# Kernel optimization log

Hardware: AMD Instinct MI355X
Metric: run time of the kernel (lower is better)

## Reference

```python
import jax, jax.numpy as jnp
import numpy as np

T, N, E = 4, 20000, 320000
F_IN, EH, NH, GH, OUT = 12, 32, 64, 64, 1
NUM_LAYERS = 2
EB_IN = (EH + 2 * NH) * 2 + GH  # 384
NB_IN = 2 * NH + 2 * EH + GH    # 256
GB_IN = NH + EH + GH            # 160


def setup_inputs() -> dict:
    key = jax.random.key(0)
    ks = jax.random.split(key, 24)
    f32 = jnp.float32
    def w(k, fan_in, shape):
        return jax.random.normal(k, shape, f32) * (1.0 / np.sqrt(fan_in))
    return {
        "node_attr": jax.random.normal(ks[0], (T, N, F_IN), f32),
        "edge_attr": jax.random.normal(ks[1], (T, E, 1), f32),
        "edge_index": jax.random.randint(ks[2], (2, E), 0, N, jnp.int32),
        "sp_L_vals": jax.random.normal(ks[3], (E,), f32),
        "global_attr": jax.random.normal(ks[4], (1, GH), f32),
        "coeff": jnp.full((1,), 0.1, f32),
        "W_ee": w(ks[5], 1, (1, EH)), "b_ee": jnp.zeros((EH,), f32),
        "W_ne": w(ks[6], F_IN, (F_IN, NH)), "b_ne": jnp.zeros((NH,), f32),
        "W_eb": w(ks[7], EB_IN, (EB_IN, EH)), "b_eb": jnp.zeros((EH,), f32),
        "W_nb": w(ks[8], NB_IN, (NB_IN, NH)), "b_nb": jnp.zeros((NH,), f32),
        "W_gb": w(ks[9], GB_IN, (GB_IN, GH)), "b_gb": jnp.zeros((GH,), f32),
        "W_nd1": w(ks[10], NH, (NH, NH)), "b_nd1": jnp.zeros((NH,), f32),
        "W_nd2": w(ks[11], NH, (NH, OUT)), "b_nd2": jnp.zeros((OUT,), f32),
    }


def _forward(node_attr, edge_attr, edge_index, sp_L_vals, global_attr, coeff,
             W_ee, b_ee, W_ne, b_ne, W_eb, b_eb, W_nb, b_nb, W_gb, b_gb,
             W_nd1, b_nd1, W_nd2, b_nd2):
    relu = jax.nn.relu
    s, r = edge_index[0], edge_index[1]
    seg = lambda v, idx: jax.ops.segment_sum(v, idx, num_segments=N)
    c = coeff[0]

    # encoders
    x_enc = relu(node_attr @ W_ne + b_ne)   # [T,N,NH]
    e_enc = relu(edge_attr @ W_ee + b_ee)   # [T,E,EH]

    def run_gn(xT, eT, g0):
        # recurrent GN core over processing steps; hidden (h_x,h_e,h_g) starts at zeros
        def step(carry, inp):
            h_x, h_e, h_g = carry
            x_in, e_in = inp
            gE = jnp.broadcast_to(h_g, (E, GH))
            # EdgeBlock: [edge_in, edge_h, sender_in, sender_h, recv_in, recv_h, global]
            edge_cat = jnp.concatenate(
                [e_in, h_e, x_in[s], h_x[s], x_in[r], h_x[r], gE], axis=-1)
            e_new = relu(edge_cat @ W_eb + b_eb)              # [E,EH]
            sent = seg(e_new, s)                              # scatter_add by sender
            recv = seg(e_new, r)                              # scatter_add by receiver
            gN = jnp.broadcast_to(h_g, (N, GH))
            node_cat = jnp.concatenate([x_in, h_x, sent, recv, gN], axis=-1)
            x_new = relu(node_cat @ W_nb + b_nb)              # [N,NH]
            # GlobalBlock: scatter_mean == plain mean (single graph)
            g_cat = jnp.concatenate(
                [x_new.mean(0, keepdims=True), e_new.mean(0, keepdims=True), h_g], axis=-1)
            g_new = relu(g_cat @ W_gb + b_gb)                 # [1,GH]
            # physics terms (pde='diff'): time derivative = state update,
            # spatial derivative = coeff * (graph-Laplacian action via sp_L edge weights)
            t_der = x_new - h_x
            s_der = c * seg(sp_L_vals[:, None] * (x_new[s] - x_new[r]), r)
            return (x_new, e_new, g_new), (x_new, e_new, g_new, t_der, s_der)
        carry0 = (jnp.zeros((N, NH), jnp.float32), jnp.zeros((E, EH), jnp.float32), g0)
        _, ys = jax.lax.scan(step, carry0, (xT, eT))
        return ys  # xs[T,N,NH], es[T,E,EH], gs[T,1,GH], td[T,N,NH], sd[T,N,NH]

    xs, es, gs, td, sd = run_gn(x_enc, e_enc, global_attr)
    x_pre = x_enc
    for _ in range(NUM_LAYERS - 1):
        x_res = xs + x_pre          # residual node state feeds next GN layer
        x_pre = x_res
        xs, es, gs, td, sd = run_gn(x_res, es, gs[0])

    x_final = xs + x_pre            # add_residual=True final residual
    h = relu(x_final @ W_nd1 + b_nd1)
    out_nodes = h @ W_nd2 + b_nd2   # [T,N,OUT]
    return out_nodes, td, sd


def reference(node_attr, edge_attr, edge_index, sp_L_vals, global_attr, coeff,
              W_ee, b_ee, W_ne, b_ne, W_eb, b_eb, W_nb, b_nb, W_gb, b_gb,
              W_nd1, b_nd1, W_nd2, b_nd2):
    return _forward(node_attr, edge_attr, edge_index, sp_L_vals, global_attr, coeff,
                    W_ee, b_ee, W_ne, b_ne, W_eb, b_eb, W_nb, b_nb, W_gb, b_gb,
                    W_nd1, b_nd1, W_nd2, b_nd2)
```

## Files before the change

### kernel.cpp

```cpp
#include <hip/hip_runtime.h>


typedef __attribute__((ext_vector_type(8))) short s16x8;
typedef __attribute__((ext_vector_type(4))) float f32x4;

#define T_STEPS 4
#define NN 20000
#define NP 20224
#define NE 320000

__device__ __forceinline__ float bf2f(unsigned short h){
  return __uint_as_float(((unsigned)h)<<16);
}
__device__ __forceinline__ unsigned short f2bf(float f){
  unsigned u = __float_as_uint(f);
  return (unsigned short)((u + 0x7fffu + ((u>>16)&1u)) >> 16);
}
__device__ __forceinline__ float loadIn(const void* p, size_t i, int bf){
  return bf ? bf2f(((const unsigned short*)p)[i]) : ((const float*)p)[i];
}
__device__ __forceinline__ void storeOut(void* o, size_t i, float v, int bf){
  if(bf) ((unsigned short*)o)[i] = f2bf(v);
  else   ((float*)o)[i] = v;
}
__device__ __forceinline__ void load8(const float* __restrict__ p, float* v){
  const float4* q4 = (const float4*)p;
  float4 a = q4[0], b = q4[1];
  v[0]=a.x; v[1]=a.y; v[2]=a.z; v[3]=a.w;
  v[4]=b.x; v[5]=b.y; v[6]=b.z; v[7]=b.w;
}
__device__ __forceinline__ int4 pack8(const float* v){
  unsigned p0 = (unsigned)f2bf(v[0]) | ((unsigned)f2bf(v[1])<<16);
  unsigned p1 = (unsigned)f2bf(v[2]) | ((unsigned)f2bf(v[3])<<16);
  unsigned p2 = (unsigned)f2bf(v[4]) | ((unsigned)f2bf(v[5])<<16);
  unsigned p3 = (unsigned)f2bf(v[6]) | ((unsigned)f2bf(v[7])<<16);
  return make_int4((int)p0,(int)p1,(int)p2,(int)p3);
}
__device__ __forceinline__ void unp8(int4 w, float* a){
  unsigned x;
  x=(unsigned)w.x; a[0]=__uint_as_float(x<<16); a[1]=__uint_as_float(x&0xffff0000u);
  x=(unsigned)w.y; a[2]=__uint_as_float(x<<16); a[3]=__uint_as_float(x&0xffff0000u);
  x=(unsigned)w.z; a[4]=__uint_as_float(x<<16); a[5]=__uint_as_float(x&0xffff0000u);
  x=(unsigned)w.w; a[6]=__uint_as_float(x<<16); a[7]=__uint_as_float(x&0xffff0000u);
}

union I4S8 { int4 i; s16x8 s; };

__global__ void probe_kernel(const void* coeff_in, int* flagp, float* coeff_f){
  unsigned short u = ((const unsigned short*)coeff_in)[0];
  float as_bf = bf2f(u);
  int f = (fabsf(as_bf - 0.1f) < 0.02f) ? 1 : 0;
  *flagp = f;
  *coeff_f = f ? as_bf : ((const float*)coeff_in)[0];
}

struct ConvJob { const void* src; float* dst; int n; };
struct ConvJobs { ConvJob j[16]; int cnt; };

__global__ void conv_kernel(ConvJobs jobs, const int* flagp, float* z, int zn){
  int bf = *flagp;
  int tid = blockIdx.x*blockDim.x + threadIdx.x;
  int stride = gridDim.x*blockDim.x;
  for(int q=0;q<jobs.cnt;q++){
    const void* s = jobs.j[q].src; float* d = jobs.j[q].dst; int n = jobs.j[q].n;
    for(int i=tid;i<n;i+=stride) d[i] = loadIn(s, i, bf);
  }
  for(int i=tid;i<zn;i+=stride) z[i]=0.f;
}

__global__ void csr_hist(const int* __restrict__ ei, int* deg_s, int* deg_r,
                         unsigned short* __restrict__ rank_s,
                         unsigned short* __restrict__ rank_r){
  int e = blockIdx.x*256+threadIdx.x;
  rank_s[e] = (unsigned short)atomicAdd(&deg_s[ei[e]],1);
  rank_r[e] = (unsigned short)atomicAdd(&deg_r[ei[NE+e]],1);
}

__global__ void csr_scan(const int* __restrict__ deg_s, int* __restrict__ off_s,
                         const int* __restrict__ deg_r, int* __restrict__ off_r){
  const int CH = NP/256;
  const int* deg = blockIdx.x ? deg_r : deg_s;
  int* off = blockIdx.x ? off_r : off_s;
  int t = threadIdx.x;
  int base = t*CH;
  int s = 0;
  #pragma unroll 8
  for(int i=0;i<CH;i++) s += deg[base+i];
  int lane = t & 63, w = t >> 6;
  int x = s;
  #pragma unroll
  for(int o=1;o<64;o<<=1){
    int y = __shfl_up(x, o, 64);
    if(lane >= o) x += y;
  }
  __shared__ int wtot[4];
  if(lane==63) wtot[w] = x;
  __syncthreads();
  int wbase = 0;
  #pragma unroll
  for(int k=0;k<3;k++) if(k<w) wbase += wtot[k];
  int acc = wbase + x - s;
  #pragma unroll 8
  for(int i=0;i<CH;i++){
    off[base+i]=acc; acc+=deg[base+i];
  }
  if(t==255) off[NN]=acc;
}

__global__ void csr_fill(const int* __restrict__ ei,
                         const int* __restrict__ s_off, const int* __restrict__ r_off,
                         const unsigned short* __restrict__ rank_s,
                         const unsigned short* __restrict__ rank_r,
                         int* __restrict__ csr_s, int* __restrict__ csr_r,
                         int2* __restrict__ sr2,
                         const void* __restrict__ spL, float* __restrict__ spL_p,
                         const int* flagp){
  int e = blockIdx.x*256+threadIdx.x;
  int s = ei[e], r = ei[NE+e];
  int p = r_off[r] + rank_r[e];
  sr2[p] = make_int2(s,r);
  csr_r[p] = e;
  csr_s[s_off[s]+rank_s[e]] = p;
  spL_p[p] = loadIn(spL, e, *flagp);
}

__global__ void pack_w_kernel(const void* __restrict__ W,
                              unsigned short* __restrict__ P, int KW, int NT,
                              const int* flagp){
  int bf = *flagp;
  int idx = blockIdx.x*blockDim.x + threadIdx.x;
  int total = NT*KW*512;
  if(idx>=total) return;
  int j = idx & 7;
  int lane = (idx>>3) & 63;
  int rest = idx >> 9;
  int kw = rest % KW;
  int nt = rest / KW;
  int k = kw*32 + (lane>>4)*8 + j;
  int n = nt*16 + (lane&15);
  P[idx] = f2bf(loadIn(W, (size_t)k*(NT*16) + n, bf));
}

__global__ void node_enc_kernel(const void* __restrict__ na,
                                const float* __restrict__ W, const float* __restrict__ b,
                                unsigned short* __restrict__ xA, const int* flagp){
  __shared__ float arow[4][12];
  int bf = *flagp;
  int lane = threadIdx.x & 63, nl = threadIdx.x >> 6;
  int row = blockIdx.x*4 + nl;
  if(lane<12) arow[nl][lane] = loadIn(na, (size_t)row*12+lane, bf);
  __syncthreads();
  float acc = b[lane];
  #pragma unroll
  for(int k=0;k<12;k++) acc += arow[nl][k]*W[k*64+lane];
  xA[(size_t)row*64+lane] = f2bf(fmaxf(acc,0.f));
}

__global__ __launch_bounds__(256,4) void edge_block_mfma(
  const int2* __restrict__ sr2,
  const unsigned short* __restrict__ x_in,
  const unsigned short* __restrict__ h_x,
  const void* __restrict__ e_attr,
  int e_attr_off,
  const int* __restrict__ inv,
  const unsigned short* __restrict__ e_in,
  const unsigned short* __restrict__ h_e,
  const float* __restrict__ g,
  const float* __restrict__ W_ee, const float* __restrict__ b_ee,
  const unsigned short* __restrict__ Wp,
  const float* __restrict__ b_eb,
  unsigned short* __restrict__ e_out,
  float* __restrict__ partial_e,
  const int* flagp)
{
  const int tid = threadIdx.x;
  const int lane = tid&63;
  const int q = lane>>4, m16 = lane&15;
  const int pair = blockIdx.x*4 + (tid>>6);
  const int e0 = pair*32;
  const int eg0 = e0 + m16, eg1 = e0 + 16 + m16;
  const int2 sr0 = sr2[eg0], sr1 = sr2[eg1];
  const int o8 = q*8;
  const int4 z4 = make_int4(0,0,0,0);

  I4S8 A0[12], A1[12];
  if(e_attr){
    int bf = *flagp;
    float a0v = loadIn(e_attr, (size_t)e_attr_off + inv[eg0], bf);
    float a1v = loadIn(e_attr, (size_t)e_attr_off + inv[eg1], bf);
    float v[8];
    #pragma unroll
    for(int j=0;j<8;j++) v[j] = fmaxf(a0v*W_ee[o8+j]+b_ee[o8+j], 0.f);
    A0[0].i = pack8(v);
    #pragma unroll
    for(int j=0;j<8;j++) v[j] = fmaxf(a1v*W_ee[o8+j]+b_ee[o8+j], 0.f);
    A1[0].i = pack8(v);
  } else {
    A0[0].i = ((const int4*)(e_in + (size_t)eg0*32))[q];
    A1[0].i = ((const int4*)(e_in + (size_t)eg1*32))[q];
  }
  A0[1].i = h_e ? ((const int4*)(h_e + (size_t)eg0*32))[q] : z4;
  A1[1].i = h_e ? ((const int4*)(h_e + (size_t)eg1*32))[q] : z4;
  { const int4* p0 = (const int4*)(x_in + (size_t)sr0.x*64);
    const int4* p1 = (const int4*)(x_in + (size_t)sr1.x*64);
    A0[2].i = p0[q]; A1[2].i = p1[q];
    A0[3].i = p0[4+q]; A1[3].i = p1[4+q]; }
  if(h_x){
    const int4* p0 = (const int4*)(h_x + (size_t)sr0.x*64);
    const int4* p1 = (const int4*)(h_x + (size_t)sr1.x*64);
    A0[4].i = p0[q]; A1[4].i = p1[q];
    A0[5].i = p0[4+q]; A1[5].i = p1[4+q];
  } else { A0[4].i=z4; A1[4].i=z4; A0[5].i=z4; A1[5].i=z4; }
  { const int4* p0 = (const int4*)(x_in + (size_t)sr0.y*64);
    const int4* p1 = (const int4*)(x_in + (size_t)sr1.y*64);
    A0[6].i = p0[q]; A1[6].i = p1[q];
    A0[7].i = p0[4+q]; A1[7].i = p1[4+q]; }
  if(h_x){
    const int4* p0 = (const int4*)(h_x + (size_t)sr0.y*64);
    const int4* p1 = (const int4*)(h_x + (size_t)sr1.y*64);
    A0[8].i = p0[q]; A1[8].i = p1[q];
    A0[9].i = p0[4+q]; A1[9].i = p1[4+q];
  } else { A0[8].i=z4; A1[8].i=z4; A0[9].i=z4; A1[9].i=z4; }
  { float v[8];
    load8(g + o8, v);      A0[10].i = pack8(v); A1[10].i = A0[10].i;
    load8(g + 32 + o8, v); A0[11].i = pack8(v); A1[11].i = A0[11].i; }

  f32x4 a00={0.f,0.f,0.f,0.f}, a01={0.f,0.f,0.f,0.f};
  f32x4 a10={0.f,0.f,0.f,0.f}, a11={0.f,0.f,0.f,0.f};
  #pragma unroll
  for(int kw=0;kw<12;kw++){
    s16x8 b0 = *(const s16x8*)(Wp + (size_t)(kw*64 + lane)*8);
    s16x8 b1 = *(const s16x8*)(Wp + (size_t)((12+kw)*64 + lane)*8);
    a00 = __builtin_amdgcn_mfma_f32_16x16x32_bf16(A0[kw].s, b0, a00, 0,0,0);
    a01 = __builtin_amdgcn_mfma_f32_16x16x32_bf16(A0[kw].s, b1, a01, 0,0,0);
    a10 = __builtin_amdgcn_mfma_f32_16x16x32_bf16(A1[kw].s, b0, a10, 0,0,0);
    a11 = __builtin_amdgcn_mfma_f32_16x16x32_bf16(A1[kw].s, b1, a11, 0,0,0);
  }

  float pe0=0.f, pe1=0.f;
  const float bb0 = b_eb[m16], bb1 = b_eb[16+m16];
  #pragma unroll
  for(int r=0;r<4;r++){
    int eg0m = e0 + q*4 + r;
    int eg1m = eg0m + 16;
    float v00 = fmaxf(a00[r]+bb0, 0.f);
    float v01 = fmaxf(a01[r]+bb1, 0.f);
    float v10 = fmaxf(a10[r]+bb0, 0.f);
    float v11 = fmaxf(a11[r]+bb1, 0.f);
    e_out[(size_t)eg0m*32+m16]    = f2bf(v00);
    e_out[(size_t)eg0m*32+16+m16] = f2bf(v01);
    e_out[(size_t)eg1m*32+m16]    = f2bf(v10);
    e_out[(size_t)eg1m*32+16+m16] = f2bf(v11);
    pe0 += v00+v10; pe1 += v01+v11;
  }
  pe0 += __shfl_xor(pe0,16,64); pe0 += __shfl_xor(pe0,32,64);
  pe1 += __shfl_xor(pe1,16,64); pe1 += __shfl_xor(pe1,32,64);
  if(q==0){
    int slot = blockIdx.x & 63;
    atomicAdd(&partial_e[slot*32+m16],    pe0);
    atomicAdd(&partial_e[slot*32+16+m16], pe1);
  }
}

__global__ void aggregate_kernel(const unsigned short* __restrict__ e_new,
  const int* __restrict__ s_off, const int* __restrict__ csr_s,
  const int* __restrict__ r_off,
  unsigned short* __restrict__ sentB, unsigned short* __restrict__ recvB)
{
  int node = blockIdx.x*4 + (threadIdx.x>>6);
  int lane = threadIdx.x & 63;
  int c4 = (lane & 7) * 4;
  int jr = lane >> 3;
  float s0=0.f,s1=0.f,s2=0.f,s3=0.f;
  float r0=0.f,r1=0.f,r2=0.f,r3=0.f;
  {
    int beg = s_off[node], end = s_off[node+1];
    for(int i=beg+jr; i<end; i+=8){
      uint2 w = *(const uint2*)(e_new + (size_t)csr_s[i]*32 + c4);
      s0 += __uint_as_float(w.x<<16);
      s1 += __uint_as_float(w.x&0xffff0000u);
      s2 += __uint_as_float(w.y<<16);
      s3 += __uint_as_float(w.y&0xffff0000u);
    }
  }
  {
    int beg = r_off[node], end = r_off[node+1];
    for(int i=beg+jr; i<end; i+=8){
      uint2 w = *(const uint2*)(e_new + (size_t)i*32 + c4);
      r0 += __uint_as_float(w.x<<16);
      r1 += __uint_as_float(w.x&0xffff0000u);
      r2 += __uint_as_float(w.y<<16);
      r3 += __uint_as_float(w.y&0xffff0000u);
    }
  }
  #pragma unroll
  for(int o=8;o<64;o<<=1){
    s0 += __shfl_xor(s0,o,64); s1 += __shfl_xor(s1,o,64);
    s2 += __shfl_xor(s2,o,64); s3 += __shfl_xor(s3,o,64);
    r0 += __shfl_xor(r0,o,64); r1 += __shfl_xor(r1,o,64);
    r2 += __shfl_xor(r2,o,64); r3 += __shfl_xor(r3,o,64);
  }
  if(jr==0){
    unsigned slo = (unsigned)f2bf(s0) | ((unsigned)f2bf(s1)<<16);
    unsigned shi = (unsigned)f2bf(s2) | ((unsigned)f2bf(s3)<<16);
    unsigned rlo = (unsigned)f2bf(r0) | ((unsigned)f2bf(r1)<<16);
    unsigned rhi = (unsigned)f2bf(r2) | ((unsigned)f2bf(r3)<<16);
    *(uint2*)(sentB + (size_t)node*32 + c4) = make_uint2(slo,shi);
    *(uint2*)(recvB + (size_t)node*32 + c4) = make_uint2(rlo,rhi);
  }
}

__global__ __launch_bounds__(256) void node_block_mfma(
  const unsigned short* __restrict__ x_in, const unsigned short* __restrict__ h_x,
  const unsigned short* __restrict__ sentB, const unsigned short* __restrict__ recvB,
  const float* __restrict__ g,
  const unsigned short* __restrict__ Wp,
  const float* __restrict__ b_nb,
  unsigned short* __restrict__ x_out, float* __restrict__ partial_x,
  void* __restrict__ out_base, size_t td_off, int has_td,
  const int* flagp)
{
  const int tid = threadIdx.x, lane = tid&63;
  const int q = lane>>4, m16 = lane&15;
  const int tile = blockIdx.x*4 + (tid>>6);
  if(tile >= NN/16) return;
  const int n0 = tile*16;
  const int ng = n0+m16;
  const int o8 = q*8;
  const int4 z4 = make_int4(0,0,0,0);

  I4S8 A[8];
  { const int4* xp = (const int4*)(x_in + (size_t)ng*64);
    A[0].i = xp[q]; A[1].i = xp[4+q]; }
  if(h_x){ const int4* hp = (const int4*)(h_x + (size_t)ng*64);
    A[2].i = hp[q]; A[3].i = hp[4+q];
  } else { A[2].i = z4; A[3].i = z4; }
  A[4].i = ((const int4*)(sentB + (size_t)ng*32))[q];
  A[5].i = ((const int4*)(recvB + (size_t)ng*32))[q];
  { float v[8];
    load8(g + o8, v);      A[6].i = pack8(v);
    load8(g + 32 + o8, v); A[7].i = pack8(v); }

  f32x4 acc[4];
  #pragma unroll
  for(int nt=0;nt<4;nt++) acc[nt] = (f32x4){0.f,0.f,0.f,0.f};
  #pragma unroll
  for(int kw=0;kw<8;kw++){
    #pragma unroll
    for(int nt=0;nt<4;nt++){
      s16x8 b = *(const s16x8*)(Wp + (size_t)((nt*8+kw)*64 + lane)*8);
      acc[nt] = __builtin_amdgcn_mfma_f32_16x16x32_bf16(A[kw].s, b, acc[nt], 0,0,0);
    }
  }

  int bf = has_td ? *flagp : 0;
  float ps[4] = {0.f,0.f,0.f,0.f};
  #pragma unroll
  for(int r=0;r<4;r++){
    int nodeg = n0 + q*4 + r;
    #pragma unroll
    for(int nt=0;nt<4;nt++){
      int col = nt*16 + m16;
      float vv = fmaxf(acc[nt][r] + b_nb[col], 0.f);
      x_out[(size_t)nodeg*64+col] = f2bf(vv);
      if(has_td){
        float hxv = h_x ? bf2f(h_x[(size_t)nodeg*64+col]) : 0.f;
        storeOut(out_base, td_off + (size_t)nodeg*64+col, vv - hxv, bf);
      }
      ps[nt] += vv;
    }
  }
  #pragma unroll
  for(int nt=0;nt<4;nt++){
    ps[nt] += __shfl_xor(ps[nt],16,64);
    ps[nt] += __shfl_xor(ps[nt],32,64);
  }
  if(q==0){
    int slot = blockIdx.x & 63;
    #pragma unroll
    for(int nt=0;nt<4;nt++)
      atomicAdd(&partial_x[slot*64 + nt*16 + m16], ps[nt]);
  }
}

__global__ void global_block_kernel(float* __restrict__ partial_x,
  float* __restrict__ partial_e, const float* __restrict__ h_g,
  const float* __restrict__ W_gb, const float* __restrict__ b_gb,
  float* __restrict__ g_out)
{
  __shared__ float gcat[160];
  __shared__ float red[4][64];
  int tid = threadIdx.x;
  if(tid<64){
    float sx = 0.f;
    #pragma unroll 8
    for(int i=0;i<64;i++) sx += partial_x[i*64+tid];
    gcat[tid] = sx * (1.0f/(float)NN);
  } else if(tid<96){
    int j = tid-64;
    float se = 0.f;
    #pragma unroll 8
    for(int i=0;i<64;i++) se += partial_e[i*32+j];
    gcat[64+j] = se * (1.0f/(float)NE);
  } else if(tid<160){
    gcat[tid] = h_g[tid-96];
  }
  __syncthreads();
  int j = tid&63, c = tid>>6;
  float acc = 0.f;
  #pragma unroll 8
  for(int k=c*40;k<c*40+40;k++) acc += gcat[k]*W_gb[k*64+j];
  red[c][j] = acc;
  __syncthreads();
  for(int i=tid;i<2048;i+=256) partial_e[i]=0.f;
  for(int i=tid;i<4096;i+=256) partial_x[i]=0.f;
  if(tid<64){
    float a = red[0][tid]+red[1][tid]+red[2][tid]+red[3][tid] + b_gb[tid];
    g_out[tid] = fmaxf(a, 0.f);
  }
}

__global__ void sder_csr_kernel(const int2* __restrict__ sr2,
  const float* __restrict__ spL_p, const unsigned short* __restrict__ x_new,
  const int* __restrict__ r_off,
  const float* __restrict__ coeff, void* __restrict__ out_base, size_t off,
  const int* flagp)
{
  int bf = *flagp;
  int lane = threadIdx.x&63, nl = threadIdx.x>>6;
  int node = blockIdx.x*4+nl;
  float xn = bf2f(x_new[(size_t)node*64+lane]);
  float a0=0.f, a1=0.f, a2=0.f, a3=0.f;
  int beg = r_off[node], end = r_off[node+1];
  int i = beg;
  for(; i+4<=end; i+=4){
    float w1 = spL_p[i],   w2 = spL_p[i+1];
    float w3 = spL_p[i+2], w4 = spL_p[i+3];
    int s1 = sr2[i].x, s2 = sr2[i+1].x, s3 = sr2[i+2].x, s4 = sr2[i+3].x;
    a0 += w1*(bf2f(x_new[(size_t)s1*64+lane])-xn);
    a1 += w2*(bf2f(x_new[(size_t)s2*64+lane])-xn);
    a2 += w3*(bf2f(x_new[(size_t)s3*64+lane])-xn);
    a3 += w4*(bf2f(x_new[(size_t)s4*64+lane])-xn);
  }
  for(; i<end; i++){
    float w1 = spL_p[i];
    a0 += w1*(bf2f(x_new[(size_t)sr2[i].x*64+lane])-xn);
  }
  storeOut(out_base, off + (size_t)node*64+lane, coeff[0]*((a0+a1)+(a2+a3)), bf);
}

__global__ void add_bf16_kernel(const unsigned short* __restrict__ a,
  const unsigned short* __restrict__ b, unsigned short* __restrict__ c, int n){
  int i = blockIdx.x*blockDim.x+threadIdx.x;
  int stride = gridDim.x*blockDim.x;
  for(;i<n;i+=stride) c[i] = f2bf(bf2f(a[i])+bf2f(b[i]));
}

__global__ __launch_bounds__(256) void decoder_kernel(
  const unsigned short* __restrict__ xs, const unsigned short* __restrict__ xr,
  const unsigned short* __restrict__ WpD,
  const float* __restrict__ b1, const float* __restrict__ W2,
  const float* __restrict__ b2,
  void* __restrict__ out_base, const int* flagp)
{
  const int tid=threadIdx.x, lane=tid&63;
  const int q=lane>>4, m16=lane&15;
  const int tile = blockIdx.x*4 + (tid>>6);
  const int row0 = tile*16;
  const int rg = row0 + m16;

  I4S8 A[2];
  #pragma unroll
  for(int kw=0;kw<2;kw++){
    int4 xa = ((const int4*)(xs + (size_t)rg*64 + kw*32))[q];
    int4 xb = ((const int4*)(xr + (size_t)rg*64 + kw*32))[q];
    float va[8], vb[8], v[8];
    unp8(xa, va); unp8(xb, vb);
    #pragma unroll
    for(int j=0;j<8;j++) v[j] = va[j]+vb[j];
    A[kw].i = pack8(v);
  }

  f32x4 acc[4];
  #pragma unroll
  for(int nt=0;nt<4;nt++) acc[nt] = (f32x4){0.f,0.f,0.f,0.f};
  #pragma unroll
  for(int kw=0;kw<2;kw++){
    #pragma unroll
    for(int nt=0;nt<4;nt++){
      s16x8 b = *(const s16x8*)(WpD + (size_t)((nt*2+kw)*64 + lane)*8);
      acc[nt] = __builtin_amdgcn_mfma_f32_16x16x32_bf16(A[kw].s, b, acc[nt], 0,0,0);
    }
  }

  float val[4];
  #pragma unroll
  for(int r=0;r<4;r++){
    float s = 0.f;
    #pragma unroll
    for(int nt=0;nt<4;nt++){
      int col = nt*16 + m16;
      s += fmaxf(acc[nt][r] + b1[col], 0.f) * W2[col];
    }
    val[r] = s;
  }
  #pragma unroll
  for(int o=1;o<16;o<<=1){
    #pragma unroll
    for(int r=0;r<4;r++) val[r] += __shfl_xor(val[r], o, 64);
  }
  if(m16==0){
    int bf = *flagp;
    float bb = b2[0];
    #pragma unroll
    for(int r=0;r<4;r++)
      storeOut(out_base, (size_t)(row0 + q*4 + r), val[r] + bb, bf);
  }
}

extern "C" void kernel_launch(void* const* d_in, const int* in_sizes, int n_in,
                              void* d_out, int out_size, void* d_ws, size_t ws_size,
                              hipStream_t stream){
  const void* node_attr = d_in[0];
  const void* edge_attr = d_in[1];
  const int*  ei        = (const int*)d_in[2];
  const void* spL       = d_in[3];
  const void* gattr     = d_in[4];
  const void* coeff_in  = d_in[5];
  const void* W_ee_in = d_in[6];  const void* b_ee_in = d_in[7];
  const void* W_ne_in = d_in[8];  const void* b_ne_in = d_in[9];
  const void* W_eb_in = d_in[10]; const void* b_eb_in = d_in[11];
  const void* W_nb_in = d_in[12]; const void* b_nb_in = d_in[13];
  const void* W_gb_in = d_in[14]; const void* b_gb_in = d_in[15];
  const void* W_nd1_in= d_in[16]; const void* b_nd1_in= d_in[17];
  const void* W_nd2_in= d_in[18]; const void* b_nd2_in= d_in[19];

  float* ws = (float*)d_ws;
  float* W_ee_f = ws;             float* b_ee_f = W_ee_f+32;
  float* W_ne_f = b_ee_f+32;      float* b_ne_f = W_ne_f+768;
  float* W_gb_f = b_ne_f+64;      float* b_gb_f = W_gb_f+10240;
  float* W_nd1_f= b_gb_f+64;      float* b_nd1_f= W_nd1_f+4096;
  float* W_nd2_f= b_nd1_f+64;     float* b_nd2_f= W_nd2_f+64;
  float* b_eb_f = b_nd2_f+1;      float* b_nb_f = b_eb_f+32;
  float* coeff_f= b_nb_f+64;
  int*   flagp  = (int*)(ws + 15523);
  float* gbuf   = ws + 15524;
  float* part_e = ws + 16100;
  float* part_x = part_e + 2048;
  int*   deg_s  = (int*)(part_x + 4096);
  int*   deg_r  = deg_s + NP;
  int*   s_off  = deg_r + NP;
  int*   r_off  = s_off + NP+1;
  unsigned short* rank_s = (unsigned short*)(r_off + NP+1);
  unsigned short* rank_r = rank_s + NE;
  int*   csr_s  = (int*)(rank_r + NE);
  int*   csr_r  = csr_s + NE;
  float* spL_p  = (float*)(csr_r + NE);
  size_t iend   = (size_t)((int*)(spL_p + NE) - (int*)ws);
  iend = (iend + 3) & ~(size_t)3;
  int2*  sr2    = (int2*)(ws + iend);
  unsigned short* sentB = (unsigned short*)(sr2 + NE);
  unsigned short* recvB = sentB + (size_t)NN*32;
  unsigned short* eBuf  = recvB + (size_t)NN*32;
  unsigned short* xA    = eBuf + (size_t)T_STEPS*NE*32;
  unsigned short* xB    = xA + (size_t)T_STEPS*NN*64;
  unsigned short* xC    = xB + (size_t)T_STEPS*NN*64;
  unsigned short* WpE   = xC + (size_t)T_STEPS*NN*64;
  unsigned short* WpN   = WpE + 12288;
  unsigned short* WpD   = WpN + 16384;

  probe_kernel<<<1,1,0,stream>>>(coeff_in, flagp, coeff_f);

  ConvJobs jobs; int c=0;
  auto add=[&](const void* s, float* d, int n){ jobs.j[c].src=s; jobs.j[c].dst=d; jobs.j[c].n=n; c++; };
  add(W_ee_in,W_ee_f,32);   add(b_ee_in,b_ee_f,32);
  add(W_ne_in,W_ne_f,768);  add(b_ne_in,b_ne_f,64);
  add(W_gb_in,W_gb_f,10240);add(b_gb_in,b_gb_f,64);
  add(W_nd1_in,W_nd1_f,4096);add(b_nd1_in,b_nd1_f,64);
  add(W_nd2_in,W_nd2_f,64); add(b_nd2_in,b_nd2_f,1);
  add(b_eb_in,b_eb_f,32);   add(b_nb_in,b_nb_f,64);
  add(gattr,gbuf,64);
  jobs.cnt=c;
  conv_kernel<<<64,256,0,stream>>>(jobs, flagp, part_e, 2048+4096+2*NP);

  csr_hist<<<NE/256,256,0,stream>>>(ei, deg_s, deg_r, rank_s, rank_r);
  csr_scan<<<2,256,0,stream>>>(deg_s, s_off, deg_r, r_off);
  csr_fill<<<NE/256,256,0,stream>>>(ei, s_off, r_off, rank_s, rank_r,
      csr_s, csr_r, sr2, spL, spL_p, flagp);

  pack_w_kernel<<<48,256,0,stream>>>(W_eb_in, WpE, 12, 2, flagp);
  pack_w_kernel<<<64,256,0,stream>>>(W_nb_in, WpN, 8, 4, flagp);
  pack_w_kernel<<<16,256,0,stream>>>(W_nd1_in, WpD, 2, 4, flagp);

  node_enc_kernel<<<T_STEPS*NN/4,256,0,stream>>>(node_attr, W_ne_f, b_ne_f, xA, flagp);

  const size_t td_base = (size_t)T_STEPS*NN;
  const size_t sd_base = td_base + (size_t)T_STEPS*NN*64;

  for(int layer=0; layer<2; layer++){
    for(int t=0;t<T_STEPS;t++){
      const unsigned short* x_in = (layer==0? xA : xC) + (size_t)t*NN*64;
      const unsigned short* h_x  = (t>0)? xB + (size_t)(t-1)*NN*64 : nullptr;
      const unsigned short* h_e  = (t>0)? eBuf + (size_t)(t-1)*NE*32 : nullptr;
      const float* gptr = (layer==0)? gbuf + t*64
                                    : (t==0? gbuf+1*64 : gbuf+(4+t)*64);
      float*       gout = (layer==0)? gbuf+(1+t)*64 : gbuf+(5+t)*64;
      const void*  eat  = (layer==0)? edge_attr : nullptr;
      const unsigned short* e_in = (layer==0)? nullptr : eBuf + (size_t)t*NE*32;
      unsigned short*       e_out= eBuf + (size_t)t*NE*32;

      edge_block_mfma<<<NE/128,256,0,stream>>>(sr2, x_in, h_x, eat, t*NE, csr_r,
          e_in, h_e, gptr, W_ee_f, b_ee_f, WpE, b_eb_f, e_out, part_e, flagp);

      aggregate_kernel<<<NN/4,256,0,stream>>>(e_out, s_off, csr_s, r_off,
          sentB, recvB);

      unsigned short* x_out = xB + (size_t)t*NN*64;
      size_t td_off = td_base + (size_t)t*NN*64;
      node_block_mfma<<<(NN/16+3)/4,256,0,stream>>>(x_in, h_x, sentB, recvB, gptr,
          WpN, b_nb_f, x_out, part_x, d_out, td_off, (layer==1)?1:0, flagp);

      global_block_kernel<<<1,256,0,stream>>>(part_x, part_e, gptr, W_gb_f, b_gb_f, gout);

      if(layer==1){
        sder_csr_kernel<<<NN/4,256,0,stream>>>(sr2, spL_p, x_out, r_off,
            coeff_f, d_out, sd_base + (size_t)t*NN*64, flagp);
      }
    }
    if(layer==0){
      add_bf16_kernel<<<2048,256,0,stream>>>(xA, xB, xC, T_STEPS*NN*64);
    }
  }

  decoder_kernel<<<(T_STEPS*NN/16+3)/4,256,0,stream>>>(xB, xC, WpD,
      b_nd1_f, W_nd2_f, b_nd2_f, d_out, flagp);
}
```

Before: 779.9 us.

## Fuse setup kernels, global block into node block, and residual add into node output

Folds the coefficient probe into the conversion kernel and merges CSR fill, weight packing and node encoding into one multi-role launch. The per-step global block becomes a last-block-done tail of the node block kernel, using an atomic counter and atomic loads of the partial sums. The layer-0 residual add is written directly from the node block epilogue instead of a separate elementwise pass. This removes many small launches and one full pass over node states, at the cost of extra branching and an atomic completion handshake that must be memory-ordered correctly.

```diff
diff --git a/kernel.cpp b/kernel.cpp
--- a/kernel.cpp
+++ b/kernel.cpp
@@ -46,20 +46,16 @@
 
 union I4S8 { int4 i; s16x8 s; };
 
-__global__ void probe_kernel(const void* coeff_in, int* flagp, float* coeff_f){
+struct ConvJob { const void* src; float* dst; int n; };
+struct ConvJobs { ConvJob j[16]; int cnt; };
+
+__global__ void conv_kernel(ConvJobs jobs, const void* coeff_in, int* flagp,
+                            float* coeff_f, float* z, int zn){
   unsigned short u = ((const unsigned short*)coeff_in)[0];
   float as_bf = bf2f(u);
-  int f = (fabsf(as_bf - 0.1f) < 0.02f) ? 1 : 0;
-  *flagp = f;
-  *coeff_f = f ? as_bf : ((const float*)coeff_in)[0];
-}
-
-struct ConvJob { const void* src; float* dst; int n; };
-struct ConvJobs { ConvJob j[16]; int cnt; };
-
-__global__ void conv_kernel(ConvJobs jobs, const int* flagp, float* z, int zn){
-  int bf = *flagp;
+  int bf = (fabsf(as_bf - 0.1f) < 0.02f) ? 1 : 0;
   int tid = blockIdx.x*blockDim.x + threadIdx.x;
+  if(tid==0){ *flagp = bf; *coeff_f = bf ? as_bf : ((const float*)coeff_in)[0]; }
   int stride = gridDim.x*blockDim.x;
   for(int q=0;q<jobs.cnt;q++){
     const void* s = jobs.j[q].src; float* d = jobs.j[q].dst; int n = jobs.j[q].n;
@@ -107,53 +103,56 @@
   if(t==255) off[NN]=acc;
 }
 
-__global__ void csr_fill(const int* __restrict__ ei,
-                         const int* __restrict__ s_off, const int* __restrict__ r_off,
-                         const unsigned short* __restrict__ rank_s,
-                         const unsigned short* __restrict__ rank_r,
-                         int* __restrict__ csr_s, int* __restrict__ csr_r,
-                         int2* __restrict__ sr2,
-                         const void* __restrict__ spL, float* __restrict__ spL_p,
-                         const int* flagp){
-  int e = blockIdx.x*256+threadIdx.x;
-  int s = ei[e], r = ei[NE+e];
-  int p = r_off[r] + rank_r[e];
-  sr2[p] = make_int2(s,r);
-  csr_r[p] = e;
-  csr_s[s_off[s]+rank_s[e]] = p;
-  spL_p[p] = loadIn(spL, e, *flagp);
-}
-
-__global__ void pack_w_kernel(const void* __restrict__ W,
-                              unsigned short* __restrict__ P, int KW, int NT,
-                              const int* flagp){
-  int bf = *flagp;
-  int idx = blockIdx.x*blockDim.x + threadIdx.x;
-  int total = NT*KW*512;
-  if(idx>=total) return;
-  int j = idx & 7;
-  int lane = (idx>>3) & 63;
-  int rest = idx >> 9;
-  int kw = rest % KW;
-  int nt = rest / KW;
-  int k = kw*32 + (lane>>4)*8 + j;
-  int n = nt*16 + (lane&15);
-  P[idx] = f2bf(loadIn(W, (size_t)k*(NT*16) + n, bf));
-}
-
-__global__ void node_enc_kernel(const void* __restrict__ na,
-                                const float* __restrict__ W, const float* __restrict__ b,
-                                unsigned short* __restrict__ xA, const int* flagp){
+__global__ void fill_pack_enc_kernel(
+  const int* __restrict__ ei,
+  const int* __restrict__ s_off, const int* __restrict__ r_off,
+  const unsigned short* __restrict__ rank_s,
+  const unsigned short* __restrict__ rank_r,
+  int* __restrict__ csr_s, int* __restrict__ csr_r, int2* __restrict__ sr2,
+  const void* __restrict__ spL, float* __restrict__ spL_p,
+  const void* __restrict__ W_eb_in, const void* __restrict__ W_nb_in,
+  const void* __restrict__ W_nd1_in,
+  unsigned short* __restrict__ WpE, unsigned short* __restrict__ WpN,
+  unsigned short* __restrict__ WpD,
+  const void* __restrict__ na, const float* __restrict__ W_ne,
+  const float* __restrict__ b_ne, unsigned short* __restrict__ xA,
+  const int* flagp)
+{
   __shared__ float arow[4][12];
-  int bf = *flagp;
-  int lane = threadIdx.x & 63, nl = threadIdx.x >> 6;
-  int row = blockIdx.x*4 + nl;
-  if(lane<12) arow[nl][lane] = loadIn(na, (size_t)row*12+lane, bf);
-  __syncthreads();
-  float acc = b[lane];
-  #pragma unroll
-  for(int k=0;k<12;k++) acc += arow[nl][k]*W[k*64+lane];
-  xA[(size_t)row*64+lane] = f2bf(fmaxf(acc,0.f));
+  const int blk = blockIdx.x;
+  const int bf = *flagp;
+  if(blk < NE/256){
+    int e = blk*256+threadIdx.x;
+    int s = ei[e], r = ei[NE+e];
+    int p = r_off[r] + rank_r[e];
+    sr2[p] = make_int2(s,r);
+    csr_r[p] = e;
+    csr_s[s_off[s]+rank_s[e]] = p;
+    spL_p[p] = loadIn(spL, e, bf);
+  } else if(blk < NE/256 + 128){
+    int idx = (blk - NE/256)*256 + threadIdx.x;
+    const void* W; unsigned short* P; int KW, NT;
+    if(idx < 12288){ W=W_eb_in; P=WpE; KW=12; NT=2; }
+    else if(idx < 28672){ idx -= 12288; W=W_nb_in; P=WpN; KW=8; NT=4; }
+    else { idx -= 28672; W=W_nd1_in; P=WpD; KW=2; NT=4; }
+    int j = idx & 7;
+    int lane = (idx>>3) & 63;
+    int rest = idx >> 9;
+    int kw = rest % KW;
+    int nt = rest / KW;
+    int k = kw*32 + (lane>>4)*8 + j;
+    int n = nt*16 + (lane&15);
+    P[idx] = f2bf(loadIn(W, (size_t)k*(NT*16) + n, bf));
+  } else {
+    int lane = threadIdx.x & 63, nl = threadIdx.x >> 6;
+    int row = (blk - (NE/256 + 128))*4 + nl;
+    if(lane<12) arow[nl][lane] = loadIn(na, (size_t)row*12+lane, bf);
+    __syncthreads();
+    float acc = b_ne[lane];
+    #pragma unroll
+    for(int k=0;k<12;k++) acc += arow[nl][k]*W_ne[k*64+lane];
+    xA[(size_t)row*64+lane] = f2bf(fmaxf(acc,0.f));
+  }
 }
 
 __global__ __launch_bounds__(256,4) void edge_block_mfma(
@@ -316,101 +315,114 @@
   const float* __restrict__ g,
   const unsigned short* __restrict__ Wp,
   const float* __restrict__ b_nb,
-  unsigned short* __restrict__ x_out, float* __restrict__ partial_x,
+  unsigned short* __restrict__ x_out,
+  unsigned short* __restrict__ xres_out,
+  float* __restrict__ partial_x,
   void* __restrict__ out_base, size_t td_off, int has_td,
+  float* __restrict__ partial_e,
+  const float* __restrict__ W_gb, const float* __restrict__ b_gb,
+  float* __restrict__ g_out, int* __restrict__ cnt,
   const int* flagp)
 {
+  __shared__ int lastFlag;
+  __shared__ float gcat[160];
+  __shared__ float red[4][64];
   const int tid = threadIdx.x, lane = tid&63;
   const int q = lane>>4, m16 = lane&15;
   const int tile = blockIdx.x*4 + (tid>>6);
-  if(tile >= NN/16) return;
-  const int n0 = tile*16;
-  const int ng = n0+m16;
-  const int o8 = q*8;
-  const int4 z4 = make_int4(0,0,0,0);
-
-  I4S8 A[8];
-  { const int4* xp = (const int4*)(x_in + (size_t)ng*64);
-    A[0].i = xp[q]; A[1].i = xp[4+q]; }
-  if(h_x){ const int4* hp = (const int4*)(h_x + (size_t)ng*64);
-    A[2].i = hp[q]; A[3].i = hp[4+q];
-  } else { A[2].i = z4; A[3].i = z4; }
-  A[4].i = ((const int4*)(sentB + (size_t)ng*32))[q];
-  A[5].i = ((const int4*)(recvB + (size_t)ng*32))[q];
-  { float v[8];
-    load8(g + o8, v);      A[6].i = pack8(v);
-    load8(g + 32 + o8, v); A[7].i = pack8(v); }
-
-  f32x4 acc[4];
-  #pragma unroll
-  for(int nt=0;nt<4;nt++) acc[nt] = (f32x4){0.f,0.f,0.f,0.f};
-  #pragma unroll
-  for(int kw=0;kw<8;kw++){
+  if(tile < NN/16){
+    const int n0 = tile*16;
+    const int ng = n0+m16;
+    const int o8 = q*8;
+    const int4 z4 = make_int4(0,0,0,0);
+
+    I4S8 A[8];
+    { const int4* xp = (const int4*)(x_in + (size_t)ng*64);
+      A[0].i = xp[q]; A[1].i = xp[4+q]; }
+    if(h_x){ const int4* hp = (const int4*)(h_x + (size_t)ng*64);
+      A[2].i = hp[q]; A[3].i = hp[4+q];
+    } else { A[2].i = z4; A[3].i = z4; }
+    A[4].i = ((const int4*)(sentB + (size_t)ng*32))[q];
+    A[5].i = ((const int4*)(recvB + (size_t)ng*32))[q];
+    { float v[8];
+      load8(g + o8, v);      A[6].i = pack8(v);
+      load8(g + 32 + o8, v); A[7].i = pack8(v); }
+
+    f32x4 acc[4];
+    #pragma unroll
+    for(int nt=0;nt<4;nt++) acc[nt] = (f32x4){0.f,0.f,0.f,0.f};
+    #pragma unroll
+    for(int kw=0;kw<8;kw++){
+      #pragma unroll
+      for(int nt=0;nt<4;nt++){
+        s16x8 b = *(const s16x8*)(Wp + (size_t)((nt*8+kw)*64 + lane)*8);
+        acc[nt] = __builtin_amdgcn_mfma_f32_16x16x32_bf16(A[kw].s, b, acc[nt], 0,0,0);
+      }
+    }
+
+    int bf = has_td ? *flagp : 0;
+    float ps[4] = {0.f,0.f,0.f,0.f};
+    #pragma unroll
+    for(int r=0;r<4;r++){
+      int nodeg = n0 + q*4 + r;
+      #pragma unroll
+      for(int nt=0;nt<4;nt++){
+        int col = nt*16 + m16;
+        float vv = fmaxf(acc[nt][r] + b_nb[col], 0.f);
+        unsigned short hb = f2bf(vv);
+        x_out[(size_t)nodeg*64+col] = hb;
+        if(xres_out){
+          float xv = bf2f(x_in[(size_t)nodeg*64+col]);
+          xres_out[(size_t)nodeg*64+col] = f2bf(xv + bf2f(hb));
+        }
+        if(has_td){
+          float hxv = h_x ? bf2f(h_x[(size_t)nodeg*64+col]) : 0.f;
+          storeOut(out_base, td_off + (size_t)nodeg*64+col, vv - hxv, bf);
+        }
+        ps[nt] += vv;
+      }
+    }
     #pragma unroll
     for(int nt=0;nt<4;nt++){
-      s16x8 b = *(const s16x8*)(Wp + (size_t)((nt*8+kw)*64 + lane)*8);
-      acc[nt] = __builtin_amdgcn_mfma_f32_16x16x32_bf16(A[kw].s, b, acc[nt], 0,0,0);
-    }
-  }
-
-  int bf = has_td ? *flagp : 0;
-  float ps[4] = {0.f,0.f,0.f,0.f};
-  #pragma unroll
-  for(int r=0;r<4;r++){
-    int nodeg = n0 + q*4 + r;
-    #pragma unroll
-    for(int nt=0;nt<4;nt++){
-      int col = nt*16 + m16;
-      float vv = fmaxf(acc[nt][r] + b_nb[col], 0.f);
-      x_out[(size_t)nodeg*64+col] = f2bf(vv);
-      if(has_td){
-        float hxv = h_x ? bf2f(h_x[(size_t)nodeg*64+col]) : 0.f;
-        storeOut(out_base, td_off + (size_t)nodeg*64+col, vv - hxv, bf);
-      }
-      ps[nt] += vv;
-    }
-  }
-  #pragma unroll
-  for(int nt=0;nt<4;nt++){
-    ps[nt] += __shfl_xor(ps[nt],16,64);
-    ps[nt] += __shfl_xor(ps[nt],32,64);
-  }
-  if(q==0){
-    int slot = blockIdx.x & 63;
-    #pragma unroll
-    for(int nt=0;nt<4;nt++)
-      atomicAdd(&partial_x[slot*64 + nt*16 + m16], ps[nt]);
-  }
-}
-
-__global__ void global_block_kernel(float* __restrict__ partial_x,
-  float* __restrict__ partial_e, const float* __restrict__ h_g,
-  const float* __restrict__ W_gb, const float* __restrict__ b_gb,
-  float* __restrict__ g_out)
-{
-  __shared__ float gcat[160];
-  __shared__ float red[4][64];
-  int tid = threadIdx.x;
+      ps[nt] += __shfl_xor(ps[nt],16,64);
+      ps[nt] += __shfl_xor(ps[nt],32,64);
+    }
+    if(q==0){
+      int slot = blockIdx.x & 63;
+      #pragma unroll
+      for(int nt=0;nt<4;nt++)
+        atomicAdd(&partial_x[slot*64 + nt*16 + m16], ps[nt]);
+    }
+  }
+
+  asm volatile("s_waitcnt vmcnt(0)" ::: "memory");
+  __syncthreads();
+  if(tid==0) lastFlag = (atomicAdd(cnt,1) == (int)gridDim.x - 1) ? 1 : 0;
+  __syncthreads();
+  if(!lastFlag) return;
+
   if(tid<64){
     float sx = 0.f;
     #pragma unroll 8
-    for(int i=0;i<64;i++) sx += partial_x[i*64+tid];
+    for(int i=0;i<64;i++)
+      sx += __hip_atomic_load(&partial_x[i*64+tid], __ATOMIC_RELAXED, __HIP_MEMORY_SCOPE_AGENT);
     gcat[tid] = sx * (1.0f/(float)NN);
   } else if(tid<96){
     int j = tid-64;
     float se = 0.f;
     #pragma unroll 8
-    for(int i=0;i<64;i++) se += partial_e[i*32+j];
+    for(int i=0;i<64;i++)
+      se += __hip_atomic_load(&partial_e[i*32+j], __ATOMIC_RELAXED, __HIP_MEMORY_SCOPE_AGENT);
     gcat[64+j] = se * (1.0f/(float)NE);
   } else if(tid<160){
-    gcat[tid] = h_g[tid-96];
+    gcat[tid] = g[tid-96];
   }
   __syncthreads();
-  int j = tid&63, c = tid>>6;
-  float acc = 0.f;
+  int j = tid&63, cc = tid>>6;
+  float acc2 = 0.f;
   #pragma unroll 8
-  for(int k=c*40;k<c*40+40;k++) acc += gcat[k]*W_gb[k*64+j];
-  red[c][j] = acc;
+  for(int k=cc*40;k<cc*40+40;k++) acc2 += gcat[k]*W_gb[k*64+j];
+  red[cc][j] = acc2;
   __syncthreads();
   for(int i=tid;i<2048;i+=256) partial_e[i]=0.f;
   for(int i=tid;i<4096;i+=256) partial_x[i]=0.f;
@@ -418,6 +430,7 @@
     float a = red[0][tid]+red[1][tid]+red[2][tid]+red[3][tid] + b_gb[tid];
     g_out[tid] = fmaxf(a, 0.f);
   }
+  if(tid==0) *cnt = 0;
 }
 
 __global__ void sder_csr_kernel(const int2* __restrict__ sr2,
@@ -449,13 +462,6 @@
   storeOut(out_base, off + (size_t)node*64+lane, coeff[0]*((a0+a1)+(a2+a3)), bf);
 }
 
-__global__ void add_bf16_kernel(const unsigned short* __restrict__ a,
-  const unsigned short* __restrict__ b, unsigned short* __restrict__ c, int n){
-  int i = blockIdx.x*blockDim.x+threadIdx.x;
-  int stride = gridDim.x*blockDim.x;
-  for(;i<n;i+=stride) c[i] = f2bf(bf2f(a[i])+bf2f(b[i]));
-}
-
 __global__ __launch_bounds__(256) void decoder_kernel(
   const unsigned short* __restrict__ xs, const unsigned short* __restrict__ xr,
   const unsigned short* __restrict__ WpD,
@@ -545,7 +551,9 @@
   float* coeff_f= b_nb_f+64;
   int*   flagp  = (int*)(ws + 15523);
   float* gbuf   = ws + 15524;
-  float* part_e = ws + 16100;
+  float* zbase  = ws + 16100;
+  int*   cnt    = (int*)zbase;
+  float* part_e = zbase + 4;
   float* part_x = part_e + 2048;
   int*   deg_s  = (int*)(part_x + 4096);
   int*   deg_r  = deg_s + NP;
@@ -569,8 +577,6 @@
   unsigned short* WpN   = WpE + 12288;
   unsigned short* WpD   = WpN + 16384;
 
-  probe_kernel<<<1,1,0,stream>>>(coeff_in, flagp, coeff_f);
-
   ConvJobs jobs; int c=0;
   auto add=[&](const void* s, float* d, int n){ jobs.j[c].src=s; jobs.j[c].dst=d; jobs.j[c].n=n; c++; };
   add(W_ee_in,W_ee_f,32);   add(b_ee_in,b_ee_f,32);
@@ -581,18 +587,16 @@
   add(b_eb_in,b_eb_f,32);   add(b_nb_in,b_nb_f,64);
   add(gattr,gbuf,64);
   jobs.cnt=c;
-  conv_kernel<<<64,256,0,stream>>>(jobs, flagp, part_e, 2048+4096+2*NP);
+  conv_kernel<<<64,256,0,stream>>>(jobs, coeff_in, flagp, coeff_f,
+      zbase, 4+2048+4096+2*NP);
 
   csr_hist<<<NE/256,256,0,stream>>>(ei, deg_s, deg_r, rank_s, rank_r);
   csr_scan<<<2,256,0,stream>>>(deg_s, s_off, deg_r, r_off);
-  csr_fill<<<NE/256,256,0,stream>>>(ei, s_off, r_off, rank_s, rank_r,
-      csr_s, csr_r, sr2, spL, spL_p, flagp);
-
-  pack_w_kernel<<<48,256,0,stream>>>(W_eb_in, WpE, 12, 2, flagp);
-  pack_w_kernel<<<64,256,0,stream>>>(W_nb_in, WpN, 8, 4, flagp);
-  pack_w_kernel<<<16,256,0,stream>>>(W_nd1_in, WpD, 2, 4, flagp);
-
-  node_enc_kernel<<<T_STEPS*NN/4,256,0,stream>>>(node_attr, W_ne_f, b_ne_f, xA, flagp);
+
+  fill_pack_enc_kernel<<<NE/256 + 128 + T_STEPS*NN/4,256,0,stream>>>(
+      ei, s_off, r_off, rank_s, rank_r, csr_s, csr_r, sr2, spL, spL_p,
+      W_eb_in, W_nb_in, W_nd1_in, WpE, WpN, WpD,
+      node_attr, W_ne_f, b_ne_f, xA, flagp);
 
   const size_t td_base = (size_t)T_STEPS*NN;
   const size_t sd_base = td_base + (size_t)T_STEPS*NN*64;
@@ -610,26 +614,24 @@
       unsigned short*       e_out= eBuf + (size_t)t*NE*32;
 
       edge_block_mfma<<<NE/128,256,0,stream>>>(sr2, x_in, h_x, eat, t*NE, csr_r,
-          e_in, h_e, gptr, W_ee_f, b_ee_f, WpE, b_eb_f, e_out, part_e, flagp);
+          e_in, h_e, gptr, W_ee_f, b_ee_f, WpE, b_eb_f, e_out,
+          part_e, flagp);
 
       aggregate_kernel<<<NN/4,256,0,stream>>>(e_out, s_off, csr_s, r_off,
           sentB, recvB);
 
       unsigned short* x_out = xB + (size_t)t*NN*64;
+      unsigned short* xres  = (layer==0)? xC + (size_t)t*NN*64 : nullptr;
       size_t td_off = td_base + (size_t)t*NN*64;
       node_block_mfma<<<(NN/16+3)/4,256,0,stream>>>(x_in, h_x, sentB, recvB, gptr,
-          WpN, b_nb_f, x_out, part_x, d_out, td_off, (layer==1)?1:0, flagp);
-
-      global_block_kernel<<<1,256,0,stream>>>(part_x, part_e, gptr, W_gb_f, b_gb_f, gout);
+          WpN, b_nb_f, x_out, xres, part_x, d_out, td_off, (layer==1)?1:0,
+          part_e, W_gb_f, b_gb_f, gout, cnt, flagp);
 
       if(layer==1){
         sder_csr_kernel<<<NN/4,256,0,stream>>>(sr2, spL_p, x_out, r_off,
             coeff_f, d_out, sd_base + (size_t)t*NN*64, flagp);
       }
     }
-    if(layer==0){
-      add_bf16_kernel<<<2048,256,0,stream>>>(xA, xB, xC, T_STEPS*NN*64);
-    }
   }
 
   decoder_kernel<<<(T_STEPS*NN/16+3)/4,256,0,stream>>>(xB, xC, WpD,
```

Measured after the change: 785.3 us. About the same (+0.7%).
